# Performance work log

Measured on AMD Instinct MI355X. Metric: run time of the kernel, lower is better.

Reference implementation:

```python
import jax, jax.numpy as jnp
import numpy as np

TOP_K = 2
NUM_MOE_LAYERS = 12


def _gemma_mlp(x, gate_w, up_w, down_w):
    # GemmaMLP: down( gelu_tanh(gate(x)) * up(x) )
    g = jnp.einsum('bsh,hi->bsi', x, gate_w)
    u = jnp.einsum('bsh,hi->bsi', x, up_w)
    return jnp.einsum('bsi,ih->bsh', jax.nn.gelu(g, approximate=True) * u, down_w)


def setup_inputs() -> dict:
    key = jax.random.key(0)
    ks = jax.random.split(key, 8)
    B, S, H, I, E = 32, 256, 1024, 4096, 8  # batch, seq, hidden, intermediate, skill experts
    std = 0.02
    return {
        'x': jax.random.normal(ks[0], (B, S, H), jnp.float32),
        'router_logits': jax.random.normal(ks[1], (B, E), jnp.float32),
        'skill_gate': jax.random.normal(ks[2], (E, H, I), jnp.float32) * std,
        'skill_up': jax.random.normal(ks[3], (E, H, I), jnp.float32) * std,
        'skill_down': jax.random.normal(ks[4], (E, I, H), jnp.float32) * std,
        'shared_gate': jax.random.normal(ks[5], (H, I), jnp.float32) * std,
        'shared_up': jax.random.normal(ks[6], (H, I), jnp.float32) * std,
        'shared_down': jax.random.normal(ks[7], (I, H), jnp.float32) * std,
    }


def reference(x, router_logits, skill_gate, skill_up, skill_down,
              shared_gate, shared_up, shared_down):
    B = x.shape[0]
    E = skill_gate.shape[0]
    # top-k softmax routing (per sequence), renormalized over selected experts
    rw = jax.nn.softmax(router_logits.astype(jnp.float32), axis=-1)
    w, sel = jax.lax.top_k(rw, TOP_K)                      # [B, k]
    w = w / w.sum(axis=-1, keepdims=True)
    w = w.astype(x.dtype)
    # ScaleGradient: identity fwd, grad scaled by 1/num_moe_layers
    scale = 1.0 / NUM_MOE_LAYERS
    w = scale * w + (1.0 - scale) * jax.lax.stop_gradient(w)
    # dense combine weights [B, E]; zero weight == not routed (same math as gather/scatter)
    dense_w = jnp.zeros((B, E), x.dtype).at[jnp.arange(B)[:, None], sel].add(w)

    def step(acc, params):
        g, u, d, we = params                               # we: [B]
        return acc + we[:, None, None] * _gemma_mlp(x, g, u, d), None

    out, _ = jax.lax.scan(step, jnp.zeros_like(x),
                          (skill_gate, skill_up, skill_down, dense_w.T))
    out = out + _gemma_mlp(x, shared_gate, shared_up, shared_down)
    return out
```

## Files before the change

### kernel.cpp

```cpp
#include <hip/hip_runtime.h>

typedef __bf16 bf16x8 __attribute__((ext_vector_type(8)));
typedef float  f32x4  __attribute__((ext_vector_type(4)));

__device__ __forceinline__ unsigned short f2bf(float f) {
    unsigned u = __float_as_uint(f);
    u += 0x7fffu + ((u >> 16) & 1u);
    return (unsigned short)(u >> 16);
}

__device__ __forceinline__ void gld_lds16(const void* g, void* l) {
    __builtin_amdgcn_global_load_lds(
        (const __attribute__((address_space(1))) void*)g,
        (__attribute__((address_space(3))) void*)l,
        16, 0, 0);
}

#define WAITVM(N) asm volatile("s_waitcnt vmcnt(" #N ")" ::: "memory")
#define SB0()     __builtin_amdgcn_sched_barrier(0)
#define BAR()     __builtin_amdgcn_s_barrier()

#define NB  32
#define SQ  256
#define HD  1024
#define ID  4096
#define NEXP 8
#define PAIRS (NB * 3)

#define OFF_EID    ((size_t)0)
#define OFF_WGT    ((size_t)512)
#define OFF_XBF    ((size_t)1024)
#define OFF_GATET  (OFF_XBF   + (size_t)16777216)
#define OFF_UPT    (OFF_GATET + (size_t)75497472)
#define OFF_DOWNT  (OFF_UPT   + (size_t)75497472)
#define OFF_ACT    (OFF_DOWNT + (size_t)75497472)

__device__ int d_sord[PAIRS];

__global__ void routing_kernel(const float* __restrict__ logits,
                               int* __restrict__ eid, float* __restrict__ wgt) {
    int b = threadIdx.x;
    if (b < NB) {
        float l[NEXP];
        for (int j = 0; j < NEXP; ++j) l[j] = logits[b * NEXP + j];
        int a0 = 0;
        for (int j = 1; j < NEXP; ++j) if (l[j] > l[a0]) a0 = j;
        int a1 = -1;
        for (int j = 0; j < NEXP; ++j) {
            if (j == a0) continue;
            if (a1 < 0 || l[j] > l[a1]) a1 = j;
        }
        float w0 = 1.0f / (1.0f + expf(l[a1] - l[a0]));
        eid[b * 3 + 0] = a0;  wgt[b * 3 + 0] = w0;
        eid[b * 3 + 1] = a1;  wgt[b * 3 + 1] = 1.0f - w0;
        eid[b * 3 + 2] = NEXP; wgt[b * 3 + 2] = 1.0f;
    }
    __syncthreads();
    if (threadIdx.x == 0) {
        int cnt[NEXP + 2];
        for (int i = 0; i < NEXP + 2; ++i) cnt[i] = 0;
        for (int i = 0; i < PAIRS; ++i) cnt[eid[i] + 1]++;
        for (int e = 0; e < NEXP + 1; ++e) cnt[e + 1] += cnt[e];
        for (int i = 0; i < PAIRS; ++i) d_sord[cnt[eid[i]]++] = i;
    }
}

__global__ void xcvt_kernel(const float* __restrict__ x,
                            unsigned short* __restrict__ xb, int n4) {
    int i = blockIdx.x * 256 + threadIdx.x;
    if (i < n4) {
        float4 v = ((const float4*)x)[i];
        union { unsigned short s[4]; uint2 u; } p;
        p.s[0] = f2bf(v.x); p.s[1] = f2bf(v.y);
        p.s[2] = f2bf(v.z); p.s[3] = f2bf(v.w);
        ((uint2*)xb)[i] = p.u;
    }
}

__global__ void transpose_cvt(const float* __restrict__ skill,
                              const float* __restrict__ shared_m,
                              unsigned short* __restrict__ out, int R, int C) {
    const int e = blockIdx.z;
    const float* src = (e < NEXP) ? (skill + (size_t)e * R * C) : shared_m;
    unsigned short* dst = out + (size_t)e * R * C;
    const int c0 = blockIdx.x * 64;
    const int r0 = blockIdx.y * 64;
    __shared__ unsigned short t[64][66];
    const int tid = threadIdx.x;
    const int lr = tid >> 4;
    const int lc = (tid & 15) * 4;
    for (int it = 0; it < 4; ++it) {
        int r = lr + it * 16;
        float4 v = *(const float4*)(src + (size_t)(r0 + r) * C + c0 + lc);
        t[r][lc + 0] = f2bf(v.x);
        t[r][lc + 1] = f2bf(v.y);
        t[r][lc + 2] = f2bf(v.z);
        t[r][lc + 3] = f2bf(v.w);
    }
    __syncthreads();
    const int oc = tid >> 2;
    const int k0 = (tid & 3) * 16;
    unsigned int pk[8];
    for (int j = 0; j < 8; ++j) {
        unsigned int lo = t[k0 + 2 * j + 0][oc];
        unsigned int hi = t[k0 + 2 * j + 1][oc];
        pk[j] = lo | (hi << 16);
    }
    unsigned short* dp = dst + (size_t)(c0 + oc) * R + r0 + k0;
    ((uint4*)dp)[0] = make_uint4(pk[0], pk[1], pk[2], pk[3]);
    ((uint4*)dp)[1] = make_uint4(pk[4], pk[5], pk[6], pk[7]);
}

#define LDFRAGS(KH, MB)                                                      \
    _Pragma("unroll") for (int i2 = 0; i2 < 4; ++i2)                         \
        av[i2] = *(const bf16x8*)(Lc + (KH) + rdA + ((MB) + i2) * 512);
#define LDBFRAGS(KH)                                                         \
    _Pragma("unroll") for (int i2 = 0; i2 < 4; ++i2)                         \
        bv[i2] = *(const bf16x8*)(Lc + (KH) + rdB + i2 * 512);
#define DOMFMA(MB)                                                           \
    __builtin_amdgcn_s_setprio(1);                                           \
    _Pragma("unroll") for (int mi = 0; mi < 4; ++mi)                         \
        _Pragma("unroll") for (int ni = 0; ni < 4; ++ni)                     \
            acc[(MB) + mi][ni] = __builtin_amdgcn_mfma_f32_16x16x32_bf16(    \
                av[mi], bv[ni], acc[(MB) + mi][ni], 0, 0, 0);                \
    __builtin_amdgcn_s_setprio(0);

__global__ __launch_bounds__(512, 2) void stage1_gateup(
    const unsigned short* __restrict__ xbf,
    const unsigned short* __restrict__ gateT,
    const unsigned short* __restrict__ upT,
    const int* __restrict__ eid, const float* __restrict__ wgt,
    unsigned short* __restrict__ act)
{
    extern __shared__ unsigned short lds[];

    const int bid = blockIdx.x;
    const int g   = bid & 7;
    const int r0_ = bid >> 3;
    const int sg  = r0_ >> 7;
    const int rr  = r0_ & 127;
    const int nt  = rr >> 2;
    const int pi  = rr & 3;
    const int p   = d_sord[g * 12 + sg * 4 + pi];
    const int b   = p / 3;
    const int e   = eid[p];
    const float wS = wgt[p];

    const int tid  = threadIdx.x;
    const int wv   = tid >> 6;
    const int lane = tid & 63;
    const int wr   = wv >> 2;
    const int wc   = wv & 3;
    const int lrow = lane & 15;
    const int chunk = lane >> 4;
    const int lr4  = lane >> 2;

    const int stc8 = (((lane & 3) ^ ((lane >> 2) & 3)) << 3);
    const int dA   = (wv * 2) * 512;

    const unsigned short* pa[2];
    const unsigned short* pb[2];
#pragma unroll
    for (int q = 0; q < 2; ++q) {
        const int seg = wv * 2 + q;
        pa[q] = xbf + ((size_t)(b * SQ + seg * 16 + lr4)) * HD + stc8;
        const int s    = (seg >> 1) & 1;
        const int icol = nt * 128 + (seg >> 2) * 32 + (seg & 1) * 16 + lr4;
        pb[q] = (s ? upT : gateT) + ((size_t)e * ID + icol) * HD + stc8;
    }

    const int rdA = (wr * 128 + lrow) * 32 + ((chunk ^ (lrow & 3)) << 3);
    const int rdB = 16384 + (wc * 64 + lrow) * 32 + ((chunk ^ (lrow & 3)) << 3);

    f32x4 acc[8][4];
#pragma unroll
    for (int i = 0; i < 8; ++i)
#pragma unroll
        for (int j = 0; j < 4; ++j) acc[i][j] = (f32x4)0.f;

    {
        unsigned short* L0 = lds;
        gld_lds16(pa[0],      L0 +          dA);
        gld_lds16(pa[1],      L0 +          dA + 512);
        gld_lds16(pb[0],      L0 + 16384 +  dA);
        gld_lds16(pb[1],      L0 + 16384 +  dA + 512);
        gld_lds16(pa[0] + 32, L0 +  8192 +  dA);
        gld_lds16(pa[1] + 32, L0 +  8192 +  dA + 512);
        gld_lds16(pb[0] + 32, L0 + 24576 +  dA);
        gld_lds16(pb[1] + 32, L0 + 24576 +  dA + 512);
        SB0(); WAITVM(4); SB0();
        BAR();
    }

    const int NT = HD / 64;
#pragma unroll 1
    for (int t = 0; t < NT; ++t) {
        unsigned short* Lc = lds + (t & 1) * 32768;
        unsigned short* Ln = lds + ((t & 1) ^ 1) * 32768;
        const bool pf = (t + 1 < NT);
        const int kof = (t + 1) * 64;
        bf16x8 av[4], bv[4];

        LDFRAGS(0, 0); LDBFRAGS(0);
        if (pf) { gld_lds16(pa[0] + kof, Ln + dA); gld_lds16(pa[1] + kof, Ln + dA + 512); }
        BAR();
        DOMFMA(0);
        BAR();

        LDFRAGS(0, 4);
        if (pf) { gld_lds16(pb[0] + kof, Ln + 16384 + dA); gld_lds16(pb[1] + kof, Ln + 16384 + dA + 512); }
        SB0();
        if (pf) { WAITVM(4); } else { WAITVM(0); }
        SB0();
        BAR();
        DOMFMA(4);
        BAR();

        LDFRAGS(8192, 0); LDBFRAGS(8192);
        if (pf) { gld_lds16(pa[0] + kof + 32, Ln + 8192 + dA); gld_lds16(pa[1] + kof + 32, Ln + 8192 + dA + 512); }
        BAR();
        DOMFMA(0);
        BAR();

        LDFRAGS(8192, 4);
        if (pf) {
            gld_lds16(pb[0] + kof + 32, Ln + 24576 + dA);
            gld_lds16(pb[1] + kof + 32, Ln + 24576 + dA + 512);
            SB0(); WAITVM(4); SB0();
        }
        BAR();
        DOMFMA(4);
        BAR();
    }

    unsigned short* actp = act + (size_t)p * (SQ * ID);
    const int rb = wr * 128 + (chunk << 2);
    const int cb = nt * 128 + wc * 32 + lrow;
#pragma unroll
    for (int mf = 0; mf < 8; ++mf)
#pragma unroll
        for (int pp = 0; pp < 2; ++pp)
#pragma unroll
            for (int r2 = 0; r2 < 4; ++r2) {
                float gv = acc[mf][pp][r2];
                float uv = acc[mf][pp + 2][r2];
                float t2 = -1.5957691216057308f * gv * (1.0f + 0.044715f * gv * gv);
                float h  = __fdividef(gv, 1.0f + __expf(t2)) * uv * wS;
                actp[(size_t)(rb + mf * 16 + r2) * ID + cb + pp * 16] = f2bf(h);
            }
}

__global__ __launch_bounds__(512, 2) void stage2_down(
    const unsigned short* __restrict__ act,
    const unsigned short* __restrict__ downT,
    const int* __restrict__ eid,
    float* __restrict__ out,
    float* __restrict__ part1)
{
    extern __shared__ unsigned short lds[];

    const int lid = blockIdx.x;
    const int sw  = (lid & 7) * 32 + (lid >> 3);
    const int z   = sw >> 7;
    const int q7  = sw & 127;
    const int b   = q7 >> 2;
    const int ntH = q7 & 3;
    const int b3  = b * 3;
    const int e0 = eid[b3], e1 = eid[b3 + 1], e2 = eid[b3 + 2];

    const int tid  = threadIdx.x;
    const int wv   = tid >> 6;
    const int lane = tid & 63;
    const int wr   = wv >> 2;
    const int wc   = wv & 3;
    const int lrow = lane & 15;
    const int chunk = lane >> 4;
    const int lr4  = lane >> 2;
    const int stc8 = (((lane & 3) ^ ((lane >> 2) & 3)) << 3);
    const int dA   = (wv * 2) * 512;

    const int rdA = (wr * 128 + lrow) * 32 + ((chunk ^ (lrow & 3)) << 3);
    const int rdB = 16384 + (wc * 64 + lrow) * 32 + ((chunk ^ (lrow & 3)) << 3);

    f32x4 acc[8][4];
#pragma unroll
    for (int i = 0; i < 8; ++i)
#pragma unroll
        for (int j = 0; j < 4; ++j) acc[i][j] = (f32x4)0.f;

    auto mksrc = [&](int gk, const unsigned short*& a0, const unsigned short*& a1,
                     const unsigned short*& b0, const unsigned short*& b1) {
        const int slot = gk >> 6;
        const int i0   = (gk & 63) << 6;
        const int esl  = (slot == 0) ? e0 : ((slot == 1) ? e1 : e2);
        a0 = act + ((size_t)((b3 + slot) * SQ) + wv * 32 + lr4) * ID + i0 + stc8;
        a1 = a0 + (size_t)16 * ID;
        b0 = downT + ((size_t)esl * HD + ntH * 256 + wv * 32 + lr4) * ID + i0 + stc8;
        b1 = b0 + (size_t)16 * ID;
    };

    {
        const unsigned short *a0, *a1, *b0, *b1;
        mksrc(z * 96, a0, a1, b0, b1);
        unsigned short* L0 = lds;
        gld_lds16(a0,      L0 +          dA);
        gld_lds16(a1,      L0 +          dA + 512);
        gld_lds16(b0,      L0 + 16384 +  dA);
        gld_lds16(b1,      L0 + 16384 +  dA + 512);
        gld_lds16(a0 + 32, L0 +  8192 +  dA);
        gld_lds16(a1 + 32, L0 +  8192 +  dA + 512);
        gld_lds16(b0 + 32, L0 + 24576 +  dA);
        gld_lds16(b1 + 32, L0 + 24576 +  dA + 512);
        SB0(); WAITVM(4); SB0();
        BAR();
    }

    const int NT = 96;
#pragma unroll 1
    for (int t = 0; t < NT; ++t) {
        unsigned short* Lc = lds + (t & 1) * 32768;
        unsigned short* Ln = lds + ((t & 1) ^ 1) * 32768;
        const bool pf = (t + 1 < NT);
        const unsigned short *a0 = nullptr, *a1 = nullptr, *b0 = nullptr, *b1 = nullptr;
        if (pf) mksrc(z * 96 + t + 1, a0, a1, b0, b1);
        bf16x8 av[4], bv[4];

        LDFRAGS(0, 0); LDBFRAGS(0);
        if (pf) { gld_lds16(a0, Ln + dA); gld_lds16(a1, Ln + dA + 512); }
        BAR();
        DOMFMA(0);
        BAR();

        LDFRAGS(0, 4);
        if (pf) { gld_lds16(b0, Ln + 16384 + dA); gld_lds16(b1, Ln + 16384 + dA + 512); }
        SB0();
        if (pf) { WAITVM(4); } else { WAITVM(0); }
        SB0();
        BAR();
        DOMFMA(4);
        BAR();

        LDFRAGS(8192, 0); LDBFRAGS(8192);
        if (pf) { gld_lds16(a0 + 32, Ln + 8192 + dA); gld_lds16(a1 + 32, Ln + 8192 + dA + 512); }
        BAR();
        DOMFMA(0);
        BAR();

        LDFRAGS(8192, 4);
        if (pf) {
            gld_lds16(b0 + 32, Ln + 24576 + dA);
            gld_lds16(b1 + 32, Ln + 24576 + dA + 512);
            SB0(); WAITVM(4); SB0();
        }
        BAR();
        DOMFMA(4);
        BAR();
    }

    float* dst = (z == 0) ? out : part1;
    const int rb = wr * 128 + (chunk << 2);
    const int cb = ntH * 256 + wc * 64 + lrow;
#pragma unroll
    for (int mf = 0; mf < 8; ++mf)
#pragma unroll
        for (int nf = 0; nf < 4; ++nf)
#pragma unroll
            for (int r2 = 0; r2 < 4; ++r2)
                dst[((size_t)b * SQ + rb + mf * 16 + r2) * HD + cb + nf * 16] = acc[mf][nf][r2];
}

__global__ void combine_kernel(float* __restrict__ out,
                               const float* __restrict__ p1, int n4) {
    int i = blockIdx.x * 256 + threadIdx.x;
    if (i < n4) {
        float4 a = ((const float4*)out)[i];
        float4 c = ((const float4*)p1)[i];
        a.x += c.x; a.y += c.y; a.z += c.z; a.w += c.w;
        ((float4*)out)[i] = a;
    }
}

extern "C" void kernel_launch(void* const* d_in, const int* in_sizes, int n_in,
                              void* d_out, int out_size, void* d_ws, size_t ws_size,
                              hipStream_t stream) {
    const float* x        = (const float*)d_in[0];
    const float* logits   = (const float*)d_in[1];
    const float* sk_gate  = (const float*)d_in[2];
    const float* sk_up    = (const float*)d_in[3];
    const float* sk_down  = (const float*)d_in[4];
    const float* sh_gate  = (const float*)d_in[5];
    const float* sh_up    = (const float*)d_in[6];
    const float* sh_down  = (const float*)d_in[7];
    float* out = (float*)d_out;

    char* ws = (char*)d_ws;
    int*            eid   = (int*)(ws + OFF_EID);
    float*          wgt   = (float*)(ws + OFF_WGT);
    unsigned short* xbf   = (unsigned short*)(ws + OFF_XBF);
    unsigned short* gateT = (unsigned short*)(ws + OFF_GATET);
    unsigned short* upT   = (unsigned short*)(ws + OFF_UPT);
    unsigned short* downT = (unsigned short*)(ws + OFF_DOWNT);
    unsigned short* act   = (unsigned short*)(ws + OFF_ACT);
    float*          part1 = (float*)(ws + OFF_GATET);

    static int attr_set = 0;
    if (!attr_set) {
        hipFuncSetAttribute(reinterpret_cast<const void*>(stage1_gateup),
                            hipFuncAttributeMaxDynamicSharedMemorySize, 131072);
        hipFuncSetAttribute(reinterpret_cast<const void*>(stage2_down),
                            hipFuncAttributeMaxDynamicSharedMemorySize, 131072);
        attr_set = 1;
    }

    routing_kernel<<<1, 64, 0, stream>>>(logits, eid, wgt);

    const int n4 = (NB * SQ * HD) / 4;
    xcvt_kernel<<<(n4 + 255) / 256, 256, 0, stream>>>(x, xbf, n4);

    transpose_cvt<<<dim3(ID / 64, HD / 64, 9), 256, 0, stream>>>(sk_gate, sh_gate, gateT, HD, ID);
    transpose_cvt<<<dim3(ID / 64, HD / 64, 9), 256, 0, stream>>>(sk_up,   sh_up,   upT,   HD, ID);
    transpose_cvt<<<dim3(HD / 64, ID / 64, 9), 256, 0, stream>>>(sk_down, sh_down, downT, ID, HD);

    stage1_gateup<<<dim3(PAIRS * 32), 512, 131072, stream>>>(xbf, gateT, upT, eid, wgt, act);
    stage2_down<<<dim3(256), 512, 131072, stream>>>(act, downT, eid, out, part1);

    const int c4 = (NB * SQ * HD) / 4;
    combine_kernel<<<(c4 + 255) / 256, 256, 0, stream>>>(out, part1, c4);
}
```

Measured before the change: 1.125 ms.

## Register double-buffer LDS fragments and use one barrier per K-tile in GEMMs

Both GEMM main loops are restructured so LDS fragment reads for the next MFMA group are issued into alternate register buffers while the current MFMAs run. The four barriers per 64-wide K step become a single barrier with a full vmcnt/lgkmcnt wait, and all global-to-LDS prefetches for the next tile are issued early. The LDS swizzle pattern also changes, to one keyed on (lrow>>1) and lane>>3, to reduce bank conflicts. This costs more VGPRs for the extra fragment buffers and a full drain of memory operations at each tile boundary.

```diff
diff --git a/kernel.cpp b/kernel.cpp
--- a/kernel.cpp
+++ b/kernel.cpp
@@ -16,9 +16,10 @@
         16, 0, 0);
 }
 
-#define WAITVM(N) asm volatile("s_waitcnt vmcnt(" #N ")" ::: "memory")
-#define SB0()     __builtin_amdgcn_sched_barrier(0)
-#define BAR()     __builtin_amdgcn_s_barrier()
+#define WAITVM(N)  asm volatile("s_waitcnt vmcnt(" #N ")" ::: "memory")
+#define WAITLGKM() asm volatile("s_waitcnt lgkmcnt(0)" ::: "memory")
+#define SB0()      __builtin_amdgcn_sched_barrier(0)
+#define BAR()      __builtin_amdgcn_s_barrier()
 
 #define NB  32
 #define SQ  256
@@ -111,18 +112,18 @@
     ((uint4*)dp)[1] = make_uint4(pk[4], pk[5], pk[6], pk[7]);
 }
 
-#define LDFRAGS(KH, MB)                                                      \
+#define RD_A(dst, L, MB, KH)                                                 \
     _Pragma("unroll") for (int i2 = 0; i2 < 4; ++i2)                         \
-        av[i2] = *(const bf16x8*)(Lc + (KH) + rdA + ((MB) + i2) * 512);
-#define LDBFRAGS(KH)                                                         \
+        dst[i2] = *(const bf16x8*)((L) + (KH) + rdA + ((MB) + i2) * 512);
+#define RD_B(dst, L, KH)                                                     \
     _Pragma("unroll") for (int i2 = 0; i2 < 4; ++i2)                         \
-        bv[i2] = *(const bf16x8*)(Lc + (KH) + rdB + i2 * 512);
-#define DOMFMA(MB)                                                           \
+        dst[i2] = *(const bf16x8*)((L) + (KH) + rdB + i2 * 512);
+#define MF16(a, b, MB)                                                       \
     __builtin_amdgcn_s_setprio(1);                                           \
     _Pragma("unroll") for (int mi = 0; mi < 4; ++mi)                         \
         _Pragma("unroll") for (int ni = 0; ni < 4; ++ni)                     \
             acc[(MB) + mi][ni] = __builtin_amdgcn_mfma_f32_16x16x32_bf16(    \
-                av[mi], bv[ni], acc[(MB) + mi][ni], 0, 0, 0);                \
+                a[mi], b[ni], acc[(MB) + mi][ni], 0, 0, 0);                  \
     __builtin_amdgcn_s_setprio(0);
 
 __global__ __launch_bounds__(512, 2) void stage1_gateup(
@@ -155,7 +156,7 @@
     const int chunk = lane >> 4;
     const int lr4  = lane >> 2;
 
-    const int stc8 = (((lane & 3) ^ ((lane >> 2) & 3)) << 3);
+    const int stc8 = (((lane & 3) ^ ((lane >> 3) & 3)) << 3);
     const int dA   = (wv * 2) * 512;
 
     const unsigned short* pa[2];
@@ -169,8 +170,9 @@
         pb[q] = (s ? upT : gateT) + ((size_t)e * ID + icol) * HD + stc8;
     }
 
-    const int rdA = (wr * 128 + lrow) * 32 + ((chunk ^ (lrow & 3)) << 3);
-    const int rdB = 16384 + (wc * 64 + lrow) * 32 + ((chunk ^ (lrow & 3)) << 3);
+    const int csw = ((chunk ^ ((lrow >> 1) & 3)) << 3);
+    const int rdA = (wr * 128 + lrow) * 32 + csw;
+    const int rdB = 16384 + (wc * 64 + lrow) * 32 + csw;
 
     f32x4 acc[8][4];
 #pragma unroll
@@ -188,9 +190,13 @@
         gld_lds16(pa[1] + 32, L0 +  8192 +  dA + 512);
         gld_lds16(pb[0] + 32, L0 + 24576 +  dA);
         gld_lds16(pb[1] + 32, L0 + 24576 +  dA + 512);
-        SB0(); WAITVM(4); SB0();
+        SB0(); WAITVM(0); SB0();
         BAR();
-    }
+        SB0();
+    }
+
+    bf16x8 av0[4], av1[4], bv0[4], bv1[4];
+    RD_A(av0, lds, 0, 0); RD_B(bv0, lds, 0);
 
     const int NT = HD / 64;
 #pragma unroll 1
@@ -199,38 +205,45 @@
         unsigned short* Ln = lds + ((t & 1) ^ 1) * 32768;
         const bool pf = (t + 1 < NT);
         const int kof = (t + 1) * 64;
-        bf16x8 av[4], bv[4];
-
-        LDFRAGS(0, 0); LDBFRAGS(0);
-        if (pf) { gld_lds16(pa[0] + kof, Ln + dA); gld_lds16(pa[1] + kof, Ln + dA + 512); }
-        BAR();
-        DOMFMA(0);
-        BAR();
-
-        LDFRAGS(0, 4);
-        if (pf) { gld_lds16(pb[0] + kof, Ln + 16384 + dA); gld_lds16(pb[1] + kof, Ln + 16384 + dA + 512); }
-        SB0();
-        if (pf) { WAITVM(4); } else { WAITVM(0); }
-        SB0();
-        BAR();
-        DOMFMA(4);
-        BAR();
-
-        LDFRAGS(8192, 0); LDBFRAGS(8192);
-        if (pf) { gld_lds16(pa[0] + kof + 32, Ln + 8192 + dA); gld_lds16(pa[1] + kof + 32, Ln + 8192 + dA + 512); }
-        BAR();
-        DOMFMA(0);
-        BAR();
-
-        LDFRAGS(8192, 4);
+
+        RD_A(av1, Lc, 4, 0);
         if (pf) {
+            gld_lds16(pa[0] + kof, Ln + dA);
+            gld_lds16(pa[1] + kof, Ln + dA + 512);
+            gld_lds16(pb[0] + kof, Ln + 16384 + dA);
+            gld_lds16(pb[1] + kof, Ln + 16384 + dA + 512);
+        }
+        SB0();
+        MF16(av0, bv0, 0);
+        SB0();
+
+        RD_A(av0, Lc, 0, 8192);
+        RD_B(bv1, Lc, 8192);
+        if (pf) {
+            gld_lds16(pa[0] + kof + 32, Ln + 8192 + dA);
+            gld_lds16(pa[1] + kof + 32, Ln + 8192 + dA + 512);
             gld_lds16(pb[0] + kof + 32, Ln + 24576 + dA);
             gld_lds16(pb[1] + kof + 32, Ln + 24576 + dA + 512);
-            SB0(); WAITVM(4); SB0();
         }
+        SB0();
+        MF16(av1, bv0, 4);
+        SB0();
+
+        RD_A(av1, Lc, 4, 8192);
+        SB0();
+        MF16(av0, bv1, 0);
+        SB0();
+
+        WAITLGKM();
+        WAITVM(0);
+        SB0();
         BAR();
-        DOMFMA(4);
-        BAR();
+        SB0();
+
+        if (pf) { RD_A(av0, Ln, 0, 0); RD_B(bv0, Ln, 0); }
+        SB0();
+        MF16(av1, bv1, 4);
+        SB0();
     }
 
     unsigned short* actp = act + (size_t)p * (SQ * ID);
@@ -276,11 +289,12 @@
     const int lrow = lane & 15;
     const int chunk = lane >> 4;
     const int lr4  = lane >> 2;
-    const int stc8 = (((lane & 3) ^ ((lane >> 2) & 3)) << 3);
+    const int stc8 = (((lane & 3) ^ ((lane >> 3) & 3)) << 3);
     const int dA   = (wv * 2) * 512;
 
-    const int rdA = (wr * 128 + lrow) * 32 + ((chunk ^ (lrow & 3)) << 3);
-    const int rdB = 16384 + (wc * 64 + lrow) * 32 + ((chunk ^ (lrow & 3)) << 3);
+    const int csw = ((chunk ^ ((lrow >> 1) & 3)) << 3);
+    const int rdA = (wr * 128 + lrow) * 32 + csw;
+    const int rdB = 16384 + (wc * 64 + lrow) * 32 + csw;
 
     f32x4 acc[8][4];
 #pragma unroll
@@ -288,32 +302,33 @@
 #pragma unroll
         for (int j = 0; j < 4; ++j) acc[i][j] = (f32x4)0.f;
 
-    auto mksrc = [&](int gk, const unsigned short*& a0, const unsigned short*& a1,
-                     const unsigned short*& b0, const unsigned short*& b1) {
+    auto mksrc = [&](int gk, const unsigned short*& a0, const unsigned short*& b0) {
         const int slot = gk >> 6;
         const int i0   = (gk & 63) << 6;
         const int esl  = (slot == 0) ? e0 : ((slot == 1) ? e1 : e2);
         a0 = act + ((size_t)((b3 + slot) * SQ) + wv * 32 + lr4) * ID + i0 + stc8;
-        a1 = a0 + (size_t)16 * ID;
         b0 = downT + ((size_t)esl * HD + ntH * 256 + wv * 32 + lr4) * ID + i0 + stc8;
-        b1 = b0 + (size_t)16 * ID;
     };
 
     {
-        const unsigned short *a0, *a1, *b0, *b1;
-        mksrc(z * 96, a0, a1, b0, b1);
+        const unsigned short *a0, *b0;
+        mksrc(z * 96, a0, b0);
         unsigned short* L0 = lds;
-        gld_lds16(a0,      L0 +          dA);
-        gld_lds16(a1,      L0 +          dA + 512);
-        gld_lds16(b0,      L0 + 16384 +  dA);
-        gld_lds16(b1,      L0 + 16384 +  dA + 512);
-        gld_lds16(a0 + 32, L0 +  8192 +  dA);
-        gld_lds16(a1 + 32, L0 +  8192 +  dA + 512);
-        gld_lds16(b0 + 32, L0 + 24576 +  dA);
-        gld_lds16(b1 + 32, L0 + 24576 +  dA + 512);
-        SB0(); WAITVM(4); SB0();
+        gld_lds16(a0,                    L0 +          dA);
+        gld_lds16(a0 + (size_t)16 * ID,  L0 +          dA + 512);
+        gld_lds16(b0,                    L0 + 16384 +  dA);
+        gld_lds16(b0 + (size_t)16 * ID,  L0 + 16384 +  dA + 512);
+        gld_lds16(a0 + 32,                   L0 +  8192 + dA);
+        gld_lds16(a0 + (size_t)16 * ID + 32, L0 +  8192 + dA + 512);
+        gld_lds16(b0 + 32,                   L0 + 24576 + dA);
+        gld_lds16(b0 + (size_t)16 * ID + 32, L0 + 24576 + dA + 512);
+        SB0(); WAITVM(0); SB0();
         BAR();
-    }
+        SB0();
+    }
+
+    bf16x8 av0[4], av1[4], bv0[4], bv1[4];
+    RD_A(av0, lds, 0, 0); RD_B(bv0, lds, 0);
 
     const int NT = 96;
 #pragma unroll 1
@@ -321,40 +336,47 @@
         unsigned short* Lc = lds + (t & 1) * 32768;
         unsigned short* Ln = lds + ((t & 1) ^ 1) * 32768;
         const bool pf = (t + 1 < NT);
-        const unsigned short *a0 = nullptr, *a1 = nullptr, *b0 = nullptr, *b1 = nullptr;
-        if (pf) mksrc(z * 96 + t + 1, a0, a1, b0, b1);
-        bf16x8 av[4], bv[4];
-
-        LDFRAGS(0, 0); LDBFRAGS(0);
-        if (pf) { gld_lds16(a0, Ln + dA); gld_lds16(a1, Ln + dA + 512); }
+        const unsigned short *a0 = nullptr, *b0 = nullptr;
+        if (pf) mksrc(z * 96 + t + 1, a0, b0);
+
+        RD_A(av1, Lc, 4, 0);
+        if (pf) {
+            gld_lds16(a0,                   Ln + dA);
+            gld_lds16(a0 + (size_t)16 * ID, Ln + dA + 512);
+            gld_lds16(b0,                   Ln + 16384 + dA);
+            gld_lds16(b0 + (size_t)16 * ID, Ln + 16384 + dA + 512);
+        }
+        SB0();
+        MF16(av0, bv0, 0);
+        SB0();
+
+        RD_A(av0, Lc, 0, 8192);
+        RD_B(bv1, Lc, 8192);
+        if (pf) {
+            gld_lds16(a0 + 32,                   Ln + 8192 + dA);
+            gld_lds16(a0 + (size_t)16 * ID + 32, Ln + 8192 + dA + 512);
+            gld_lds16(b0 + 32,                   Ln + 24576 + dA);
+            gld_lds16(b0 + (size_t)16 * ID + 32, Ln + 24576 + dA + 512);
+        }
+        SB0();
+        MF16(av1, bv0, 4);
+        SB0();
+
+        RD_A(av1, Lc, 4, 8192);
+        SB0();
+        MF16(av0, bv1, 0);
+        SB0();
+
+        WAITLGKM();
+        WAITVM(0);
+        SB0();
         BAR();
-        DOMFMA(0);
-        BAR();
-
-        LDFRAGS(0, 4);
-        if (pf) { gld_lds16(b0, Ln + 16384 + dA); gld_lds16(b1, Ln + 16384 + dA + 512); }
-        SB0();
-        if (pf) { WAITVM(4); } else { WAITVM(0); }
-        SB0();
-        BAR();
-        DOMFMA(4);
-        BAR();
-
-        LDFRAGS(8192, 0); LDBFRAGS(8192);
-        if (pf) { gld_lds16(a0 + 32, Ln + 8192 + dA); gld_lds16(a1 + 32, Ln + 8192 + dA + 512); }
-        BAR();
-        DOMFMA(0);
-        BAR();
-
-        LDFRAGS(8192, 4);
-        if (pf) {
-            gld_lds16(b0 + 32, Ln + 24576 + dA);
-            gld_lds16(b1 + 32, Ln + 24576 + dA + 512);
-            SB0(); WAITVM(4); SB0();
-        }
-        BAR();
-        DOMFMA(4);
-        BAR();
+        SB0();
+
+        if (pf) { RD_A(av0, Ln, 0, 0); RD_B(bv0, Ln, 0); }
+        SB0();
+        MF16(av1, bv1, 4);
+        SB0();
     }
 
     float* dst = (z == 0) ? out : part1;
```

After: 1.126 ms. About the same (+0.1%).
